# Performance work log

Measured on AMD Instinct MI355X. Metric: run time of the kernel, lower is better.

The kernel has to match this reference:

```python
import jax, jax.numpy as jnp
import numpy as np

N = 65536      # total nodes
E = 1048576    # edges (no self loops)
B = 512        # graphs
NPG = 128      # nodes per graph (equal-size, contiguous batch vector)
IN = 128
H = 256
K = 64         # sort-pool k
TLD = 3 * H + 1  # total_latent_dim = (num_layers-1)*hidden + 1 = 769
OUT = 10
DENSE_IN = (K // 2 - 4) * 32  # 896


def setup_inputs() -> dict:
    key = jax.random.key(0)
    ks = jax.random.split(key, 24)
    def lin(kw, kb, fi, fo):
        s = 1.0 / np.sqrt(fi)
        return (jax.random.uniform(kw, (fi, fo), jnp.float32, -s, s),
                jax.random.uniform(kb, (fo,), jnp.float32, -s, s))
    x = jax.random.normal(ks[0], (N, IN), jnp.float32)
    edge_index = jax.random.randint(ks[1], (2, E), 0, N, jnp.int64)
    batch = (jnp.arange(N, dtype=jnp.int64) // NPG)  # contiguous equal-size graphs
    W1, b1 = lin(ks[2], ks[3], IN, H)
    W2, b2 = lin(ks[4], ks[5], H, H)
    W3, b3 = lin(ks[6], ks[7], H, H)
    W4, b4 = lin(ks[8], ks[9], H, 1)
    s1 = 1.0 / np.sqrt(1 * TLD)
    conv1_w = jax.random.uniform(ks[10], (16, 1, TLD), jnp.float32, -s1, s1)
    conv1_b = jax.random.uniform(ks[11], (16,), jnp.float32, -s1, s1)
    s2 = 1.0 / np.sqrt(16 * 5)
    conv2_w = jax.random.uniform(ks[12], (32, 16, 5), jnp.float32, -s2, s2)
    conv2_b = jax.random.uniform(ks[13], (32,), jnp.float32, -s2, s2)
    fc1_w, fc1_b = lin(ks[14], ks[15], DENSE_IN, 128)
    fc2_w, fc2_b = lin(ks[16], ks[17], 128, OUT)
    return dict(x=x, edge_index=edge_index, batch=batch,
                W1=W1, b1=b1, W2=W2, b2=b2, W3=W3, b3=b3, W4=W4, b4=b4,
                conv1_w=conv1_w, conv1_b=conv1_b, conv2_w=conv2_w, conv2_b=conv2_b,
                fc1_w=fc1_w, fc1_b=fc1_b, fc2_w=fc2_w, fc2_b=fc2_b)


def reference(x, edge_index, batch, W1, b1, W2, b2, W3, b3, W4, b4,
              conv1_w, conv1_b, conv2_w, conv2_b, fc1_w, fc1_b, fc2_w, fc2_b):
    loop = jnp.arange(N, dtype=edge_index.dtype)
    src = jnp.concatenate([edge_index[0], loop])  # self loops appended
    dst = jnp.concatenate([edge_index[1], loop])
    # deg over sources (out-degree, incl. self loop -> >=1), norm indexed by dst (as in source)
    deg = jax.ops.segment_sum(jnp.ones(src.shape[0], x.dtype), src, num_segments=N)
    norm = (1.0 / deg)[dst]  # [E+N]

    def gconv(h, W, b):
        h = h @ W + b                      # linear
        msg = h[src] * norm[:, None]       # gather + normalize
        return jnp.tanh(jax.ops.segment_sum(msg, dst, num_segments=N))  # scatter-add

    h = gconv(x, W1, b1)
    h = gconv(h, W2, b2)
    h = gconv(h, W3, b3)
    h = gconv(h, W4, b4)                   # [N, 1]

    # SortAggregation: sort nodes per graph by (last/only) channel, descending, take top-k.
    # batch is contiguous equal-size (NPG per graph) so a reshape is the segment structure.
    vals = h.reshape(B, NPG)
    top = -jnp.sort(-vals, axis=1)[:, :K]  # [B, K]

    # pad to k * total_latent_dim (as in source)
    xp = jnp.pad(top, ((0, 0), (0, K * TLD - K)))[:, None, :]  # [B, 1, K*TLD]
    y = jax.lax.conv_general_dilated(xp, conv1_w, (TLD,), 'VALID',
                                     dimension_numbers=('NCH', 'OIH', 'NCH'))
    y = jax.nn.relu(y + conv1_b[None, :, None])                # [B, 16, K]
    y = y.reshape(B, 16, K // 2, 2).max(axis=-1)               # maxpool k=2 s=2
    y = jax.lax.conv_general_dilated(y, conv2_w, (1,), 'VALID',
                                     dimension_numbers=('NCH', 'OIH', 'NCH'))
    y = jax.nn.relu(y + conv2_b[None, :, None])                # [B, 32, K//2-4]
    y = y.reshape(B, -1)
    y = jax.nn.relu(y @ fc1_w + fc1_b)                         # dropout = identity (eval)
    return y @ fc2_w + fc2_b                                   # [B, OUT]
```

## Files before the change

kernel.cpp:

```cpp
#include <hip/hip_runtime.h>

constexpr int N_NODES = 65536;
constexpr int N_EDGES = 1048576;
constexpr int NPG     = 128;
constexpr int NGRAPH  = 512;
constexpr int KTOP    = 64;

using short8 = __attribute__((ext_vector_type(8))) short;
using f32x4  = __attribute__((ext_vector_type(4))) float;

__device__ __forceinline__ float tanh_fast(float x) {
    float ex = __expf(2.0f * x);
    return 1.0f - __fdividef(2.0f, ex + 1.0f);
}
__device__ __forceinline__ unsigned bf16_rne(float f) {
    unsigned u = __float_as_uint(f);
    return (u + 0x7FFFu + ((u >> 16) & 1u)) >> 16;
}
__device__ __forceinline__ float bf16_to_f(unsigned h) {
    return __uint_as_float(h << 16);
}


__global__ __launch_bounds__(256) void init_deg_kernel(int* __restrict__ outdeg,
                                                       int* __restrict__ indeg) {
    int n = blockIdx.x * 256 + threadIdx.x;
    outdeg[n] = 1;
    indeg[n]  = 0;
}

__global__ __launch_bounds__(256) void count_kernel(const int* __restrict__ ei,
                                                    int* __restrict__ outdeg,
                                                    int* __restrict__ indeg) {
    int e = blockIdx.x * 256 + threadIdx.x;
    atomicAdd(&outdeg[ei[e]], 1);
    atomicAdd(&indeg[ei[N_EDGES + e]], 1);
}

__global__ __launch_bounds__(1024) void scan_kernel(const int* __restrict__ indeg,
                                                    int* __restrict__ row_ptr,
                                                    int* __restrict__ cursor) {
    __shared__ int sums[1024];
    int t = threadIdx.x;
    int base = t * 64;
    int ssum = 0;
    for (int i = 0; i < 64; i++) ssum += indeg[base + i];
    sums[t] = ssum;
    __syncthreads();
    for (int off = 1; off < 1024; off <<= 1) {
        int v = (t >= off) ? sums[t - off] : 0;
        __syncthreads();
        sums[t] += v;
        __syncthreads();
    }
    int run = (t == 0) ? 0 : sums[t - 1];
    for (int i = 0; i < 64; i++) {
        int v = indeg[base + i];
        row_ptr[base + i] = run;
        cursor[base + i]  = run;
        run += v;
    }
    if (t == 1023) row_ptr[N_NODES] = sums[1023];
}

__global__ __launch_bounds__(256) void norm_beta_kernel(const int* __restrict__ outdeg,
                                                        const int* __restrict__ indeg,
                                                        float* __restrict__ normv,
                                                        float* __restrict__ betav) {
    int n = blockIdx.x * 256 + threadIdx.x;
    float nm = 1.0f / (float)outdeg[n];
    normv[n] = nm;
    betav[n] = nm * (float)(indeg[n] + 1);
}

__global__ __launch_bounds__(256) void fill_kernel(const int* __restrict__ ei,
                                                   int* __restrict__ cursor,
                                                   int* __restrict__ col) {
    int e = blockIdx.x * 256 + threadIdx.x;
    int s = ei[e];
    int d = ei[N_EDGES + e];
    int p = atomicAdd(&cursor[d], 1);
    col[p] = s;
}


__global__ __launch_bounds__(256) void wsplit_kernel(const float* __restrict__ W,
                                                     ushort* __restrict__ WhT,
                                                     ushort* __restrict__ WlT, int K) {
    int idx = blockIdx.x * 256 + threadIdx.x;
    int k = idx >> 8, c = idx & 255;
    float w = W[idx];
    unsigned h = bf16_rne(w);
    unsigned l = bf16_rne(w - bf16_to_f(h));
    WhT[c * K + k] = (ushort)h;
    WlT[c * K + k] = (ushort)l;
}


__global__ __launch_bounds__(256) void agg_x_kernel(const float* __restrict__ h,
                                                    const int* __restrict__ row_ptr,
                                                    const int* __restrict__ col,
                                                    const float* __restrict__ normv,
                                                    ushort* __restrict__ Ah,
                                                    ushort* __restrict__ Al) {
    int wid  = (blockIdx.x * 256 + threadIdx.x) >> 6;
    int lane = threadIdx.x & 63;
    int e  = row_ptr[wid];
    int e1 = row_ptr[wid + 1];
    const float2* h2 = (const float2*)h;
    float2 acc = h2[(size_t)wid * 64 + lane];
    if (e + 3 < e1) {
        int i0 = col[e], i1 = col[e + 1], i2 = col[e + 2], i3 = col[e + 3];
        for (;;) {
            int en = e + 4;
            bool more = (en + 3 < e1);
            int n0 = col[en], n1 = col[en + 1], n2 = col[en + 2], n3 = col[en + 3];
            float2 v0 = h2[(size_t)i0 * 64 + lane];
            float2 v1 = h2[(size_t)i1 * 64 + lane];
            float2 v2 = h2[(size_t)i2 * 64 + lane];
            float2 v3 = h2[(size_t)i3 * 64 + lane];
            acc.x += v0.x; acc.y += v0.y;
            acc.x += v1.x; acc.y += v1.y;
            acc.x += v2.x; acc.y += v2.y;
            acc.x += v3.x; acc.y += v3.y;
            e = en;
            if (!more) break;
            i0 = n0; i1 = n1; i2 = n2; i3 = n3;
        }
    }
    for (; e < e1; e++) {
        float2 v = h2[(size_t)col[e] * 64 + lane];
        acc.x += v.x; acc.y += v.y;
    }
    float nm = normv[wid];
    float ox = acc.x * nm, oy = acc.y * nm;
    unsigned hx = bf16_rne(ox), hy = bf16_rne(oy);
    unsigned lx = bf16_rne(ox - bf16_to_f(hx));
    unsigned ly = bf16_rne(oy - bf16_to_f(hy));
    size_t base = (size_t)wid * 128 + lane * 2;
    *(unsigned*)&Ah[base] = hx | (hy << 16);
    *(unsigned*)&Al[base] = lx | (ly << 16);
}


__global__ __launch_bounds__(256) void agg_h_kernel(const ushort* __restrict__ hb,
                                                    const int* __restrict__ row_ptr,
                                                    const int* __restrict__ col,
                                                    const float* __restrict__ normv,
                                                    ushort* __restrict__ Ah,
                                                    ushort* __restrict__ Al) {
    int wid  = (blockIdx.x * 256 + threadIdx.x) >> 6;
    int lane = threadIdx.x & 63;
    int e  = row_ptr[wid];
    int e1 = row_ptr[wid + 1];
    const uint2* h2 = (const uint2*)hb;
    uint2 s = h2[(size_t)wid * 64 + lane];
    float a0 = bf16_to_f(s.x & 0xffff), a1 = bf16_to_f(s.x >> 16);
    float a2 = bf16_to_f(s.y & 0xffff), a3 = bf16_to_f(s.y >> 16);
    if (e + 3 < e1) {
        int i0 = col[e], i1 = col[e + 1], i2 = col[e + 2], i3 = col[e + 3];
        for (;;) {
            int en = e + 4;
            bool more = (en + 3 < e1);
            int n0 = col[en], n1 = col[en + 1], n2 = col[en + 2], n3 = col[en + 3];
            uint2 v0 = h2[(size_t)i0 * 64 + lane];
            uint2 v1 = h2[(size_t)i1 * 64 + lane];
            uint2 v2 = h2[(size_t)i2 * 64 + lane];
            uint2 v3 = h2[(size_t)i3 * 64 + lane];
            a0 += bf16_to_f(v0.x & 0xffff); a1 += bf16_to_f(v0.x >> 16);
            a2 += bf16_to_f(v0.y & 0xffff); a3 += bf16_to_f(v0.y >> 16);
            a0 += bf16_to_f(v1.x & 0xffff); a1 += bf16_to_f(v1.x >> 16);
            a2 += bf16_to_f(v1.y & 0xffff); a3 += bf16_to_f(v1.y >> 16);
            a0 += bf16_to_f(v2.x & 0xffff); a1 += bf16_to_f(v2.x >> 16);
            a2 += bf16_to_f(v2.y & 0xffff); a3 += bf16_to_f(v2.y >> 16);
            a0 += bf16_to_f(v3.x & 0xffff); a1 += bf16_to_f(v3.x >> 16);
            a2 += bf16_to_f(v3.y & 0xffff); a3 += bf16_to_f(v3.y >> 16);
            e = en;
            if (!more) break;
            i0 = n0; i1 = n1; i2 = n2; i3 = n3;
        }
    }
    for (; e < e1; e++) {
        uint2 v = h2[(size_t)col[e] * 64 + lane];
        a0 += bf16_to_f(v.x & 0xffff); a1 += bf16_to_f(v.x >> 16);
        a2 += bf16_to_f(v.y & 0xffff); a3 += bf16_to_f(v.y >> 16);
    }
    float nm = normv[wid];
    float ox = a0 * nm, oy = a1 * nm, oz = a2 * nm, ow = a3 * nm;
    unsigned hx = bf16_rne(ox), hy = bf16_rne(oy), hz = bf16_rne(oz), hw = bf16_rne(ow);
    unsigned lx = bf16_rne(ox - bf16_to_f(hx));
    unsigned ly = bf16_rne(oy - bf16_to_f(hy));
    unsigned lz = bf16_rne(oz - bf16_to_f(hz));
    unsigned lw = bf16_rne(ow - bf16_to_f(hw));
    size_t base = (size_t)wid * 256 + lane * 4;
    *(uint2*)&Ah[base] = make_uint2(hx | (hy << 16), hz | (hw << 16));
    *(uint2*)&Al[base] = make_uint2(lx | (ly << 16), lz | (lw << 16));
}


template <int KDIM>
__global__ __launch_bounds__(256) void gemm_mfma_tanh(const ushort* __restrict__ Ah,
                                                      const ushort* __restrict__ Al,
                                                      const ushort* __restrict__ WhT,
                                                      const ushort* __restrict__ WlT,
                                                      const float* __restrict__ bias,
                                                      const float* __restrict__ betav,
                                                      ushort* __restrict__ out) {
    __shared__ ushort Ahs[128][40], Als[128][40], Whs[128][40], Wls[128][40];
    int t    = threadIdx.x;
    int lane = t & 63, wv = t >> 6;
    int rowBase = blockIdx.x * 128;
    int colBase = blockIdx.y * 128;
    f32x4 acc[2][8] = {};

    for (int k0 = 0; k0 < KDIM; k0 += 32) {
        #pragma unroll
        for (int i = 0; i < 2; i++) {
            int idx = t + i * 256;
            int r = idx >> 2, kq = idx & 3;
            size_t g = (size_t)(rowBase + r) * KDIM + k0 + kq * 8;
            *(short8*)&Ahs[r][kq * 8] = *(const short8*)&Ah[g];
            *(short8*)&Als[r][kq * 8] = *(const short8*)&Al[g];
        }
        #pragma unroll
        for (int i = 0; i < 2; i++) {
            int idx = t + i * 256;
            int c = idx >> 2, kq = idx & 3;
            size_t g = (size_t)(colBase + c) * KDIM + k0 + kq * 8;
            *(short8*)&Whs[c][kq * 8] = *(const short8*)&WhT[g];
            *(short8*)&Wls[c][kq * 8] = *(const short8*)&WlT[g];
        }
        __syncthreads();
        int rA = wv * 32 + (lane & 15);
        int kb = (lane >> 4) * 8;
        short8 ah0 = *(const short8*)&Ahs[rA][kb];
        short8 ah1 = *(const short8*)&Ahs[rA + 16][kb];
        short8 al0 = *(const short8*)&Als[rA][kb];
        short8 al1 = *(const short8*)&Als[rA + 16][kb];
        #pragma unroll
        for (int ct = 0; ct < 8; ct++) {
            int cW = ct * 16 + (lane & 15);
            short8 wh = *(const short8*)&Whs[cW][kb];
            short8 wl = *(const short8*)&Wls[cW][kb];
            acc[0][ct] = __builtin_amdgcn_mfma_f32_16x16x32_bf16(ah0, wh, acc[0][ct], 0, 0, 0);
            acc[0][ct] = __builtin_amdgcn_mfma_f32_16x16x32_bf16(ah0, wl, acc[0][ct], 0, 0, 0);
            acc[0][ct] = __builtin_amdgcn_mfma_f32_16x16x32_bf16(al0, wh, acc[0][ct], 0, 0, 0);
            acc[1][ct] = __builtin_amdgcn_mfma_f32_16x16x32_bf16(ah1, wh, acc[1][ct], 0, 0, 0);
            acc[1][ct] = __builtin_amdgcn_mfma_f32_16x16x32_bf16(ah1, wl, acc[1][ct], 0, 0, 0);
            acc[1][ct] = __builtin_amdgcn_mfma_f32_16x16x32_bf16(al1, wh, acc[1][ct], 0, 0, 0);
        }
        __syncthreads();
    }
    int cb = colBase + (lane & 15);
    #pragma unroll
    for (int rt = 0; rt < 2; rt++) {
        int rb = rowBase + wv * 32 + rt * 16 + (lane >> 4) * 4;
        #pragma unroll
        for (int j = 0; j < 4; j++) {
            int row = rb + j;
            float bt = betav[row];
            #pragma unroll
            for (int ct = 0; ct < 8; ct++) {
                int c = cb + ct * 16;
                out[(size_t)row * 256 + c] =
                    (ushort)bf16_rne(tanh_fast(acc[rt][ct][j] + bt * bias[c]));
            }
        }
    }
}


__global__ __launch_bounds__(256) void gemv_kernel(const ushort* __restrict__ hb,
                                                   const float* __restrict__ w4,
                                                   float* __restrict__ s_lin) {
    int wid  = (blockIdx.x * 256 + threadIdx.x) >> 6;
    int lane = threadIdx.x & 63;
    const uint2* h2 = (const uint2*)hb;
    uint2 a = h2[(size_t)wid * 64 + lane];
    float4 b = ((const float4*)w4)[lane];
    float s = bf16_to_f(a.x & 0xffff) * b.x + bf16_to_f(a.x >> 16) * b.y +
              bf16_to_f(a.y & 0xffff) * b.z + bf16_to_f(a.y >> 16) * b.w;
    s += __shfl_xor(s, 32); s += __shfl_xor(s, 16); s += __shfl_xor(s, 8);
    s += __shfl_xor(s, 4);  s += __shfl_xor(s, 2);  s += __shfl_xor(s, 1);
    if (lane == 0) s_lin[wid] = s;
}

__global__ __launch_bounds__(256) void agg_scalar_kernel(const float* __restrict__ s_lin,
                                                         const int* __restrict__ row_ptr,
                                                         const int* __restrict__ col,
                                                         const float* __restrict__ normv,
                                                         const float* __restrict__ betav,
                                                         const float* __restrict__ b4,
                                                         float* __restrict__ scores) {
    int wid  = (blockIdx.x * 256 + threadIdx.x) >> 6;
    int lane = threadIdx.x & 63;
    int e0 = row_ptr[wid], e1 = row_ptr[wid + 1];
    float sum = (lane == 0) ? s_lin[wid] : 0.0f;
    for (int e = e0 + lane; e < e1; e += 64) sum += s_lin[col[e]];
    sum += __shfl_xor(sum, 32); sum += __shfl_xor(sum, 16); sum += __shfl_xor(sum, 8);
    sum += __shfl_xor(sum, 4);  sum += __shfl_xor(sum, 2);  sum += __shfl_xor(sum, 1);
    if (lane == 0) scores[wid] = tanh_fast(normv[wid] * sum + betav[wid] * b4[0]);
}


__global__ __launch_bounds__(128) void sort_kernel(const float* __restrict__ scores,
                                                   float* __restrict__ topk) {
    __shared__ float v[128];
    int b = blockIdx.x, t = threadIdx.x;
    v[t] = scores[b * NPG + t];
    __syncthreads();
    for (int k = 2; k <= 128; k <<= 1) {
        for (int j = k >> 1; j > 0; j >>= 1) {
            int ixj = t ^ j;
            if (ixj > t) {
                bool up = ((t & k) == 0);
                float a = v[t], c = v[ixj];
                bool sw = up ? (a < c) : (a > c);
                if (sw) { v[t] = c; v[ixj] = a; }
            }
            __syncthreads();
        }
    }
    if (t < KTOP) topk[b * KTOP + t] = v[t];
}


__global__ __launch_bounds__(128) void head_kernel(const float* __restrict__ topk,
                                                   const float* __restrict__ c1w,
                                                   const float* __restrict__ c1b,
                                                   const float* __restrict__ c2w,
                                                   const float* __restrict__ c2b,
                                                   const float* __restrict__ f1w,
                                                   const float* __restrict__ f1b,
                                                   const float* __restrict__ f2w,
                                                   const float* __restrict__ f2b,
                                                   float* __restrict__ out) {
    __shared__ float top[64];
    __shared__ float pool[16][32];
    __shared__ float dense[896];
    __shared__ float fc1o[128];
    int b = blockIdx.x, t = threadIdx.x;
    if (t < 64) top[t] = topk[b * KTOP + t];
    __syncthreads();
    if (t < 16) {
        float a = c1b[t];
        for (int i = 0; i < 64; i++) a += c1w[t * 769 + i] * top[i];
        float v0 = fmaxf(a, 0.0f);
        float r  = fmaxf(c1b[t], 0.0f);
        pool[t][0] = fmaxf(v0, r);
        for (int p = 1; p < 32; p++) pool[t][p] = r;
    }
    __syncthreads();
    for (int idx = t; idx < 896; idx += 128) {
        int o = idx / 28, p = idx % 28;
        float a = c2b[o];
        for (int i = 0; i < 16; i++) {
            #pragma unroll
            for (int tt = 0; tt < 5; tt++)
                a += c2w[o * 80 + i * 5 + tt] * pool[i][p + tt];
        }
        dense[idx] = fmaxf(a, 0.0f);
    }
    __syncthreads();
    {
        float a = f1b[t];
        for (int i = 0; i < 896; i++) a += f1w[i * 128 + t] * dense[i];
        fc1o[t] = fmaxf(a, 0.0f);
    }
    __syncthreads();
    if (t < 10) {
        float a = f2b[t];
        for (int i = 0; i < 128; i++) a += f2w[i * 10 + t] * fc1o[i];
        out[b * 10 + t] = a;
    }
}


extern "C" void kernel_launch(void* const* d_in, const int* in_sizes, int n_in,
                              void* d_out, int out_size, void* d_ws, size_t ws_size,
                              hipStream_t stream) {
    const float* x   = (const float*)d_in[0];
    const int*   ei  = (const int*)d_in[1];
    const float* W1 = (const float*)d_in[3];
    const float* b1 = (const float*)d_in[4];
    const float* W2 = (const float*)d_in[5];
    const float* b2 = (const float*)d_in[6];
    const float* W3 = (const float*)d_in[7];
    const float* b3 = (const float*)d_in[8];
    const float* W4 = (const float*)d_in[9];
    const float* b4 = (const float*)d_in[10];
    const float* c1w = (const float*)d_in[11];
    const float* c1b = (const float*)d_in[12];
    const float* c2w = (const float*)d_in[13];
    const float* c2b = (const float*)d_in[14];
    const float* f1w = (const float*)d_in[15];
    const float* f1b = (const float*)d_in[16];
    const float* f2w = (const float*)d_in[17];
    const float* f2b = (const float*)d_in[18];
    float* out = (float*)d_out;

    char* ws = (char*)d_ws;
    ushort* hbB  = (ushort*)ws;
    ushort* AhG  = (ushort*)(ws + ((size_t)32 << 20));
    ushort* AlG  = (ushort*)(ws + ((size_t)64 << 20));
    char* p = ws + ((size_t)96 << 20);
    auto take = [&](size_t bytes) { char* q = p; p += (bytes + 255) & ~(size_t)255; return q; };
    int*    outdeg  = (int*)take(N_NODES * 4);
    int*    indeg   = (int*)take(N_NODES * 4);
    int*    row_ptr = (int*)take((N_NODES + 1) * 4);
    int*    cursor  = (int*)take(N_NODES * 4);
    int*    col     = (int*)take(((size_t)N_EDGES + 64) * 4);
    float*  normv   = (float*)take(N_NODES * 4);
    float*  betav   = (float*)take(N_NODES * 4);
    float*  s_lin   = (float*)take(N_NODES * 4);
    float*  scores  = (float*)take(N_NODES * 4);
    float*  topk    = (float*)take(NGRAPH * KTOP * 4);
    ushort* W1hT = (ushort*)take(128 * 256 * 2);
    ushort* W1lT = (ushort*)take(128 * 256 * 2);
    ushort* W2hT = (ushort*)take(256 * 256 * 2);
    ushort* W2lT = (ushort*)take(256 * 256 * 2);
    ushort* W3hT = (ushort*)take(256 * 256 * 2);
    ushort* W3lT = (ushort*)take(256 * 256 * 2);

    init_deg_kernel<<<N_NODES / 256, 256, 0, stream>>>(outdeg, indeg);
    count_kernel<<<N_EDGES / 256, 256, 0, stream>>>(ei, outdeg, indeg);
    scan_kernel<<<1, 1024, 0, stream>>>(indeg, row_ptr, cursor);
    norm_beta_kernel<<<N_NODES / 256, 256, 0, stream>>>(outdeg, indeg, normv, betav);
    fill_kernel<<<N_EDGES / 256, 256, 0, stream>>>(ei, cursor, col);
    wsplit_kernel<<<128, 256, 0, stream>>>(W1, W1hT, W1lT, 128);
    wsplit_kernel<<<256, 256, 0, stream>>>(W2, W2hT, W2lT, 256);
    wsplit_kernel<<<256, 256, 0, stream>>>(W3, W3hT, W3lT, 256);

    dim3 gemmGrid(N_NODES / 128, 2);

    agg_x_kernel<<<N_NODES / 4, 256, 0, stream>>>(x, row_ptr, col, normv, AhG, AlG);
    gemm_mfma_tanh<128><<<gemmGrid, 256, 0, stream>>>(AhG, AlG, W1hT, W1lT, b1, betav, hbB);
    agg_h_kernel<<<N_NODES / 4, 256, 0, stream>>>(hbB, row_ptr, col, normv, AhG, AlG);
    gemm_mfma_tanh<256><<<gemmGrid, 256, 0, stream>>>(AhG, AlG, W2hT, W2lT, b2, betav, hbB);
    agg_h_kernel<<<N_NODES / 4, 256, 0, stream>>>(hbB, row_ptr, col, normv, AhG, AlG);
    gemm_mfma_tanh<256><<<gemmGrid, 256, 0, stream>>>(AhG, AlG, W3hT, W3lT, b3, betav, hbB);
    gemv_kernel<<<N_NODES / 4, 256, 0, stream>>>(hbB, W4, s_lin);
    agg_scalar_kernel<<<N_NODES / 4, 256, 0, stream>>>(s_lin, row_ptr, col, normv, betav, b4, scores);

    sort_kernel<<<NGRAPH, 128, 0, stream>>>(scores, topk);
    head_kernel<<<NGRAPH, 128, 0, stream>>>(topk, c1w, c1b, c2w, c2b, f1w, f1b, f2w, f2b, out);
}
```

Baseline: 737.6 us.

## Range-partition CSR build atomics and gather bf16 copy of x in first aggregation

The degree-count and CSR fill kernels now have each block scan a slice of edges but act only on node IDs in one of 8 ranges, so the atomics from a block land in a smaller region of memory and may get better cache locality. Each edge is read 8 times in exchange. A new kernel converts x to bf16 up front, so the first aggregation gathers half as many bytes per neighbor. This loses precision on the input features before aggregation.

```diff
diff --git a/kernel.cpp b/kernel.cpp
--- a/kernel.cpp
+++ b/kernel.cpp
@@ -5,6 +5,7 @@
 constexpr int NPG     = 128;
 constexpr int NGRAPH  = 512;
 constexpr int KTOP    = 64;
+constexpr int RSHIFT  = 13;
 
 using short8 = __attribute__((ext_vector_type(8))) short;
 using f32x4  = __attribute__((ext_vector_type(4))) float;
@@ -29,12 +30,20 @@
     indeg[n]  = 0;
 }
 
-__global__ __launch_bounds__(256) void count_kernel(const int* __restrict__ ei,
-                                                    int* __restrict__ outdeg,
-                                                    int* __restrict__ indeg) {
-    int e = blockIdx.x * 256 + threadIdx.x;
-    atomicAdd(&outdeg[ei[e]], 1);
-    atomicAdd(&indeg[ei[N_EDGES + e]], 1);
+__global__ __launch_bounds__(256) void count_range_kernel(const int* __restrict__ ei,
+                                                          int* __restrict__ outdeg,
+                                                          int* __restrict__ indeg) {
+    int r  = blockIdx.x & 7;
+    int lo = r << RSHIFT, hi = lo + (1 << RSHIFT);
+    int slice = blockIdx.x >> 3;
+    int start = slice * (N_EDGES / 256);
+    int end   = start + (N_EDGES / 256);
+    for (int i = start + threadIdx.x; i < end; i += 256) {
+        int s = ei[i];
+        int d = ei[N_EDGES + i];
+        if (s >= lo && s < hi) atomicAdd(&outdeg[s], 1);
+        if (d >= lo && d < hi) atomicAdd(&indeg[d], 1);
+    }
 }
 
 __global__ __launch_bounds__(1024) void scan_kernel(const int* __restrict__ indeg,
@@ -73,14 +82,31 @@
     betav[n] = nm * (float)(indeg[n] + 1);
 }
 
-__global__ __launch_bounds__(256) void fill_kernel(const int* __restrict__ ei,
-                                                   int* __restrict__ cursor,
-                                                   int* __restrict__ col) {
-    int e = blockIdx.x * 256 + threadIdx.x;
-    int s = ei[e];
-    int d = ei[N_EDGES + e];
-    int p = atomicAdd(&cursor[d], 1);
-    col[p] = s;
+__global__ __launch_bounds__(256) void fill_range_kernel(const int* __restrict__ ei,
+                                                         int* __restrict__ cursor,
+                                                         int* __restrict__ col) {
+    int r  = blockIdx.x & 7;
+    int lo = r << RSHIFT, hi = lo + (1 << RSHIFT);
+    int slice = blockIdx.x >> 3;
+    int start = slice * (N_EDGES / 256);
+    int end   = start + (N_EDGES / 256);
+    for (int i = start + threadIdx.x; i < end; i += 256) {
+        int d = ei[N_EDGES + i];
+        if (d >= lo && d < hi) {
+            int p = atomicAdd(&cursor[d], 1);
+            col[p] = ei[i];
+        }
+    }
+}
+
+
+__global__ __launch_bounds__(256) void xconv_kernel(const float* __restrict__ x,
+                                                    ushort* __restrict__ xb) {
+    int idx = blockIdx.x * 256 + threadIdx.x;
+    float4 v = ((const float4*)x)[idx];
+    unsigned a = bf16_rne(v.x) | (bf16_rne(v.y) << 16);
+    unsigned b = bf16_rne(v.z) | (bf16_rne(v.w) << 16);
+    ((uint2*)xb)[idx] = make_uint2(a, b);
 }
 
 
@@ -97,7 +123,7 @@
 }
 
 
-__global__ __launch_bounds__(256) void agg_x_kernel(const float* __restrict__ h,
+__global__ __launch_bounds__(256) void agg_x_kernel(const ushort* __restrict__ xb,
                                                     const int* __restrict__ row_ptr,
                                                     const int* __restrict__ col,
                                                     const float* __restrict__ normv,
@@ -107,33 +133,34 @@
     int lane = threadIdx.x & 63;
     int e  = row_ptr[wid];
     int e1 = row_ptr[wid + 1];
-    const float2* h2 = (const float2*)h;
-    float2 acc = h2[(size_t)wid * 64 + lane];
+    const uint* h1 = (const uint*)xb;
+    uint s = h1[(size_t)wid * 64 + lane];
+    float a0 = bf16_to_f(s & 0xffff), a1 = bf16_to_f(s >> 16);
     if (e + 3 < e1) {
         int i0 = col[e], i1 = col[e + 1], i2 = col[e + 2], i3 = col[e + 3];
         for (;;) {
             int en = e + 4;
             bool more = (en + 3 < e1);
             int n0 = col[en], n1 = col[en + 1], n2 = col[en + 2], n3 = col[en + 3];
-            float2 v0 = h2[(size_t)i0 * 64 + lane];
-            float2 v1 = h2[(size_t)i1 * 64 + lane];
-            float2 v2 = h2[(size_t)i2 * 64 + lane];
-            float2 v3 = h2[(size_t)i3 * 64 + lane];
-            acc.x += v0.x; acc.y += v0.y;
-            acc.x += v1.x; acc.y += v1.y;
-            acc.x += v2.x; acc.y += v2.y;
-            acc.x += v3.x; acc.y += v3.y;
+            uint v0 = h1[(size_t)i0 * 64 + lane];
+            uint v1 = h1[(size_t)i1 * 64 + lane];
+            uint v2 = h1[(size_t)i2 * 64 + lane];
+            uint v3 = h1[(size_t)i3 * 64 + lane];
+            a0 += bf16_to_f(v0 & 0xffff); a1 += bf16_to_f(v0 >> 16);
+            a0 += bf16_to_f(v1 & 0xffff); a1 += bf16_to_f(v1 >> 16);
+            a0 += bf16_to_f(v2 & 0xffff); a1 += bf16_to_f(v2 >> 16);
+            a0 += bf16_to_f(v3 & 0xffff); a1 += bf16_to_f(v3 >> 16);
             e = en;
             if (!more) break;
             i0 = n0; i1 = n1; i2 = n2; i3 = n3;
         }
     }
     for (; e < e1; e++) {
-        float2 v = h2[(size_t)col[e] * 64 + lane];
-        acc.x += v.x; acc.y += v.y;
+        uint v = h1[(size_t)col[e] * 64 + lane];
+        a0 += bf16_to_f(v & 0xffff); a1 += bf16_to_f(v >> 16);
     }
     float nm = normv[wid];
-    float ox = acc.x * nm, oy = acc.y * nm;
+    float ox = a0 * nm, oy = a1 * nm;
     unsigned hx = bf16_rne(ox), hy = bf16_rne(oy);
     unsigned lx = bf16_rne(ox - bf16_to_f(hx));
     unsigned ly = bf16_rne(oy - bf16_to_f(hy));
@@ -403,7 +430,8 @@
     ushort* hbB  = (ushort*)ws;
     ushort* AhG  = (ushort*)(ws + ((size_t)32 << 20));
     ushort* AlG  = (ushort*)(ws + ((size_t)64 << 20));
-    char* p = ws + ((size_t)96 << 20);
+    ushort* xb   = (ushort*)(ws + ((size_t)96 << 20));
+    char* p = ws + ((size_t)112 << 20);
     auto take = [&](size_t bytes) { char* q = p; p += (bytes + 255) & ~(size_t)255; return q; };
     int*    outdeg  = (int*)take(N_NODES * 4);
     int*    indeg   = (int*)take(N_NODES * 4);
@@ -423,17 +451,18 @@
     ushort* W3lT = (ushort*)take(256 * 256 * 2);
 
     init_deg_kernel<<<N_NODES / 256, 256, 0, stream>>>(outdeg, indeg);
-    count_kernel<<<N_EDGES / 256, 256, 0, stream>>>(ei, outdeg, indeg);
+    count_range_kernel<<<2048, 256, 0, stream>>>(ei, outdeg, indeg);
     scan_kernel<<<1, 1024, 0, stream>>>(indeg, row_ptr, cursor);
     norm_beta_kernel<<<N_NODES / 256, 256, 0, stream>>>(outdeg, indeg, normv, betav);
-    fill_kernel<<<N_EDGES / 256, 256, 0, stream>>>(ei, cursor, col);
+    fill_range_kernel<<<2048, 256, 0, stream>>>(ei, cursor, col);
+    xconv_kernel<<<8192, 256, 0, stream>>>(x, xb);
     wsplit_kernel<<<128, 256, 0, stream>>>(W1, W1hT, W1lT, 128);
     wsplit_kernel<<<256, 256, 0, stream>>>(W2, W2hT, W2lT, 256);
     wsplit_kernel<<<256, 256, 0, stream>>>(W3, W3hT, W3lT, 256);
 
     dim3 gemmGrid(N_NODES / 128, 2);
 
-    agg_x_kernel<<<N_NODES / 4, 256, 0, stream>>>(x, row_ptr, col, normv, AhG, AlG);
+    agg_x_kernel<<<N_NODES / 4, 256, 0, stream>>>(xb, row_ptr, col, normv, AhG, AlG);
     gemm_mfma_tanh<128><<<gemmGrid, 256, 0, stream>>>(AhG, AlG, W1hT, W1lT, b1, betav, hbB);
     agg_h_kernel<<<N_NODES / 4, 256, 0, stream>>>(hbB, row_ptr, col, normv, AhG, AlG);
     gemm_mfma_tanh<256><<<gemmGrid, 256, 0, stream>>>(AhG, AlG, W2hT, W2lT, b2, betav, hbB);
```

Result: faster. 707.2 us (-4.1%).
